# Kernel optimization log

Measured on AMD Instinct MI355X. Metric: run time of the kernel, lower is better.

Reference implementation:

```python
import jax, jax.numpy as jnp
import numpy as np

DY, DO, DI = 16, 256, 256
BS = 4096
EPS = 1e-6


def setup_inputs() -> dict:
    key = jax.random.key(0)
    k1, k2, k3, k4, k5 = jax.random.split(key, 5)
    k = 1.0 / float(np.sqrt(DY * DI))
    return {
        "x": jax.random.normal(k1, (DY * DI, BS), dtype=jnp.float32),
        "rms_params": jnp.ones((DY * DI,), dtype=jnp.float32)
        + 0.01 * jax.random.normal(k2, (DY * DI,), dtype=jnp.float32),
        "w_upper": jax.random.uniform(k3, (DY, DO, DI), minval=-k, maxval=k, dtype=jnp.float32),
        "w_lower": jax.random.uniform(k4, (DY, DO, DI), minval=-k, maxval=k, dtype=jnp.float32),
        "bias": jax.random.uniform(k5, (DY * DO,), minval=-k, maxval=k, dtype=jnp.float32),
    }


def reference(x, rms_params, w_upper, w_lower, bias):
    # x: (dy*di, bs) features-first layout, matching the torch op.
    dy, do, di = w_upper.shape
    bs = x.shape[1]
    # Per-column RMS factor (fc in the original op is shape (bs,)).
    fc = jax.lax.rsqrt(jnp.mean(x * x, axis=0) + EPS)  # (bs,)
    xn = x * rms_params[:, None] * fc[None, :]          # fused norm+scale
    xb = xn.reshape(dy, di, bs)
    # Dyadic structured matmul: upper acts on block d, lower on its paired
    # (reversed) block dy-1-d.
    up = jnp.einsum("doi,dib->dob", w_upper, xb)
    lo = jnp.einsum("doi,dib->dob", w_lower, xb[::-1])
    y = jax.nn.relu(up + lo + bias.reshape(dy, do, 1))
    return y.reshape(dy * do, bs)
```

## Files before the change

kernel.cpp:

```cpp
#include <hip/hip_runtime.h>

#define DYN 16
#define DON 256
#define DIN 256
#define BSN 4096
#define NF 4096
#define KTOT 512

typedef unsigned short u16;
typedef __attribute__((ext_vector_type(8))) short bf16x8;
typedef __attribute__((ext_vector_type(4))) float f32x4;
typedef __attribute__((ext_vector_type(4))) unsigned short u16x4;

static __device__ __forceinline__ u16 f2bf(float f) {
  unsigned u = __builtin_bit_cast(unsigned, f);
  u += 0x7fffu + ((u >> 16) & 1u);
  return (u16)(u >> 16);
}
static __device__ __forceinline__ float bf2f(u16 h) {
  unsigned u = ((unsigned)h) << 16;
  return __builtin_bit_cast(float, u);
}

__global__ __launch_bounds__(256) void k_prep_w(
    const float* __restrict__ wu, const float* __restrict__ wl,
    const float* __restrict__ rms, u16* __restrict__ aprep) {
  int e = blockIdx.x * 256 + threadIdx.x;
  int row = e >> 6;
  int k0 = (e & 63) << 3;
  int d = row >> 8;
  const float* src;
  const float* rp;
  if (k0 < 256) {
    src = wu + (size_t)row * 256 + k0;
    rp  = rms + d * 256 + k0;
  } else {
    src = wl + (size_t)row * 256 + (k0 - 256);
    rp  = rms + (DYN - 1 - d) * 256 + (k0 - 256);
  }
  float4 s0 = *reinterpret_cast<const float4*>(src);
  float4 s1 = *reinterpret_cast<const float4*>(src + 4);
  float4 r0 = *reinterpret_cast<const float4*>(rp);
  float4 r1 = *reinterpret_cast<const float4*>(rp + 4);
  bf16x8 o;
  o[0] = (short)f2bf(s0.x * r0.x); o[1] = (short)f2bf(s0.y * r0.y);
  o[2] = (short)f2bf(s0.z * r0.z); o[3] = (short)f2bf(s0.w * r0.w);
  o[4] = (short)f2bf(s1.x * r1.x); o[5] = (short)f2bf(s1.y * r1.y);
  o[6] = (short)f2bf(s1.z * r1.z); o[7] = (short)f2bf(s1.w * r1.w);
  *reinterpret_cast<bf16x8*>(aprep + (size_t)row * KTOT + k0) = o;
}

__global__ __launch_bounds__(256) void k_transpose(
    const float* __restrict__ x, u16* __restrict__ xbf,
    float* __restrict__ partial) {
  __shared__ u16 tile[128 * 132];
  const int t = threadIdx.x;
  const int bt = blockIdx.x, ft = blockIdx.y;
  const float* xb = x + (size_t)ft * 128 * BSN + bt * 128;
  const int frow = t >> 5, b4 = (t & 31) * 4;
  #pragma unroll
  for (int p = 0; p < 16; ++p) {
    int f = p * 8 + frow;
    float4 v = *reinterpret_cast<const float4*>(xb + (size_t)f * BSN + b4);
    u16x4 h;
    h[0] = f2bf(v.x); h[1] = f2bf(v.y); h[2] = f2bf(v.z); h[3] = f2bf(v.w);
    *reinterpret_cast<u16x4*>(&tile[f * 132 + b4]) = h;
  }
  __syncthreads();
  const int chunk = t & 15;
  const int bg = t >> 4;
  #pragma unroll
  for (int p = 0; p < 8; ++p) {
    int b = bg + p * 16;
    float s = 0.f;
    bf16x8 w;
    #pragma unroll
    for (int jj = 0; jj < 8; ++jj) {
      int j = (jj + chunk) & 7;
      u16 v = tile[(chunk * 8 + j) * 132 + b];
      float xv = bf2f(v);
      s += xv * xv;
      w[j] = (short)v;
    }
    *reinterpret_cast<bf16x8*>(
        xbf + (size_t)(bt * 128 + b) * NF + ft * 128 + chunk * 8) = w;
    #pragma unroll
    for (int m = 1; m < 16; m <<= 1) s += __shfl_xor(s, m, 64);
    if (chunk == 0) partial[ft * BSN + bt * 128 + b] = s;
  }
}

__global__ __launch_bounds__(256, 3) void k_gemm(
    const u16* __restrict__ aprep, const u16* __restrict__ xbf,
    const float* __restrict__ partial, const float* __restrict__ bias,
    float* __restrict__ out) {
  extern __shared__ char smem[];
  float* fcl = (float*)smem;
  u16* As = (u16*)(smem + 512);
  u16* Bs = As + 3 * 4096;
  const int bid = blockIdx.x;
  const int x8 = bid & 7, s = bid >> 3;
  const int d = (s & 1) ? (15 - x8) : x8;
  const int mt = (s >> 1) & 1;
  const int nt = s >> 2;
  const int t = threadIdx.x;
  const int wave = t >> 6, lane = t & 63;
  const int lhi = lane >> 4, llo = lane & 15;
  const int wm = wave >> 1, wn = wave & 1;
  const int arow0 = d * 256 + mt * 128;
  const int bcol0 = nt * 128;

  f32x4 acc[4][4] = {};

  auto stage = [&](int slot, int kt) {
    const int fbase = (kt < 8) ? (d * 256 + kt * 32)
                               : ((DYN - 1 - d) * 256 + (kt - 8) * 32);
    #pragma unroll
    for (int j = 0; j < 2; ++j) {
      int c = j * 256 + t;
      int cl = c ^ ((c >> 3) & 7);
      int r = cl >> 2, kc = cl & 3;
      const u16* ga = aprep + (size_t)(arow0 + r) * KTOT + kt * 32 + kc * 8;
      const u16* gb = xbf + (size_t)(bcol0 + r) * NF + fbase + kc * 8;
      unsigned lbase = (unsigned)((j * 256 + wave * 64) * 16);
      __builtin_amdgcn_global_load_lds(
          (const __attribute__((address_space(1))) unsigned int*)ga,
          (__attribute__((address_space(3))) unsigned int*)(
              (char*)&As[slot * 4096] + lbase), 16, 0, 0);
      __builtin_amdgcn_global_load_lds(
          (const __attribute__((address_space(1))) unsigned int*)gb,
          (__attribute__((address_space(3))) unsigned int*)(
              (char*)&Bs[slot * 4096] + lbase), 16, 0, 0);
    }
  };

  const int kmask = ((llo >> 1) & 7) << 4;

  stage(0, 0);
  stage(1, 1);
  if (t < 128) {
    int col = bcol0 + t;
    float fs = 0.f;
    #pragma unroll
    for (int i = 0; i < 32; ++i) fs += partial[i * BSN + col];
    fcl[t] = rsqrtf(fs * (1.0f / 4096.0f) + 1e-6f);
  }
  asm volatile("s_waitcnt vmcnt(4)\n\ts_barrier" ::: "memory");

  for (int kt = 0; kt < 16; ++kt) {
    const int slot = kt % 3;
    if (kt < 14) stage((kt + 2) % 3, kt + 2);

    bf16x8 af[4], bq[4];
    #pragma unroll
    for (int m = 0; m < 4; ++m) {
      int rowa = wm * 64 + m * 16 + llo;
      int offa = (rowa * 64 + lhi * 16) ^ kmask;
      af[m] = *reinterpret_cast<const bf16x8*>(
          (const char*)&As[slot * 4096] + offa);
    }
    #pragma unroll
    for (int n = 0; n < 4; ++n) {
      int rowb = wn * 64 + n * 16 + llo;
      int offb = (rowb * 64 + lhi * 16) ^ kmask;
      bq[n] = *reinterpret_cast<const bf16x8*>(
          (const char*)&Bs[slot * 4096] + offb);
    }
    __builtin_amdgcn_s_setprio(1);
    #pragma unroll
    for (int m = 0; m < 4; ++m)
      #pragma unroll
      for (int n = 0; n < 4; ++n)
        acc[m][n] = __builtin_amdgcn_mfma_f32_16x16x32_bf16(
            af[m], bq[n], acc[m][n], 0, 0, 0);
    __builtin_amdgcn_s_setprio(0);

    if (kt < 14) {
      asm volatile("s_waitcnt vmcnt(4)\n\ts_barrier" ::: "memory");
    } else if (kt == 14) {
      asm volatile("s_waitcnt vmcnt(0)\n\ts_barrier" ::: "memory");
    }
  }

  float fcv[4];
  #pragma unroll
  for (int n = 0; n < 4; ++n) fcv[n] = fcl[wn * 64 + n * 16 + llo];
  #pragma unroll
  for (int m = 0; m < 4; ++m) {
    int row0 = arow0 + wm * 64 + m * 16 + lhi * 4;
    float bv[4];
    #pragma unroll
    for (int r = 0; r < 4; ++r) bv[r] = bias[row0 + r];
    #pragma unroll
    for (int n = 0; n < 4; ++n) {
      int col = bcol0 + wn * 64 + n * 16 + llo;
      #pragma unroll
      for (int r = 0; r < 4; ++r) {
        float v = acc[m][n][r] * fcv[n] + bv[r];
        out[(size_t)(row0 + r) * BSN + col] = fmaxf(v, 0.f);
      }
    }
  }
}

extern "C" void kernel_launch(void* const* d_in, const int* in_sizes, int n_in,
                              void* d_out, int out_size, void* d_ws, size_t ws_size,
                              hipStream_t stream) {
  (void)in_sizes; (void)n_in; (void)out_size; (void)ws_size;
  const float* x    = (const float*)d_in[0];
  const float* rms  = (const float*)d_in[1];
  const float* wu   = (const float*)d_in[2];
  const float* wl   = (const float*)d_in[3];
  const float* bias = (const float*)d_in[4];
  float* out = (float*)d_out;

  char* ws = (char*)d_ws;
  u16* xbf      = (u16*)ws;
  u16* aprep    = (u16*)(ws + 33554432);
  float* partial = (float*)(ws + 37748736);

  k_prep_w<<<1024, 256, 0, stream>>>(wu, wl, rms, aprep);
  k_transpose<<<dim3(32, 32), 256, 0, stream>>>(x, xbf, partial);
  k_gemm<<<1024, 256, 49664, stream>>>(aprep, xbf, partial, bias, out);
}
```

Measured before the change: 57.87 us.

## Compute paired dyadic output blocks per CTA, sharing the staged x tile

Each GEMM workgroup now computes outputs for both block d and its mirror 15-d. It stages one x tile and two weight tiles per k-step, reusing the x tile across two accumulator sets. This halves x traffic per output, changes the grid from 1024 to 512 workgroups with occupancy hint 2, and enlarges LDS to triple-buffer three tiles. The epilogue is reoriented so each lane writes float4 along the batch dimension, at the cost of doubled accumulator registers.

```diff
diff --git a/kernel.cpp b/kernel.cpp
--- a/kernel.cpp
+++ b/kernel.cpp
@@ -90,115 +90,138 @@
   }
 }
 
-__global__ __launch_bounds__(256, 3) void k_gemm(
+__global__ __launch_bounds__(256, 2) void k_gemm(
     const u16* __restrict__ aprep, const u16* __restrict__ xbf,
     const float* __restrict__ partial, const float* __restrict__ bias,
     float* __restrict__ out) {
   extern __shared__ char smem[];
   float* fcl = (float*)smem;
-  u16* As = (u16*)(smem + 512);
-  u16* Bs = As + 3 * 4096;
+  u16* slots = (u16*)(smem + 512);
   const int bid = blockIdx.x;
-  const int x8 = bid & 7, s = bid >> 3;
-  const int d = (s & 1) ? (15 - x8) : x8;
-  const int mt = (s >> 1) & 1;
-  const int nt = s >> 2;
+  const int d  = bid & 7;
+  const int mt = (bid >> 3) & 1;
+  const int bt = bid >> 4;
   const int t = threadIdx.x;
   const int wave = t >> 6, lane = t & 63;
   const int lhi = lane >> 4, llo = lane & 15;
   const int wm = wave >> 1, wn = wave & 1;
-  const int arow0 = d * 256 + mt * 128;
-  const int bcol0 = nt * 128;
-
-  f32x4 acc[4][4] = {};
+  const int bb0 = bt * 128;
+  const int fr1 = d * 256 + mt * 128;
+  const int fr2 = (15 - d) * 256 + mt * 128;
+
+  f32x4 acc1[4][4] = {}, acc2[4][4] = {};
 
   auto stage = [&](int slot, int kt) {
     const int fbase = (kt < 8) ? (d * 256 + kt * 32)
-                               : ((DYN - 1 - d) * 256 + (kt - 8) * 32);
+                               : ((15 - d) * 256 + (kt - 8) * 32);
+    const int k1 = kt * 32;
+    const int k2 = (kt ^ 8) * 32;
+    char* sA  = (char*)(slots + slot * 12288);
+    char* sBd = sA + 8192;
+    char* sB2 = sA + 16384;
     #pragma unroll
     for (int j = 0; j < 2; ++j) {
       int c = j * 256 + t;
       int cl = c ^ ((c >> 3) & 7);
       int r = cl >> 2, kc = cl & 3;
-      const u16* ga = aprep + (size_t)(arow0 + r) * KTOT + kt * 32 + kc * 8;
-      const u16* gb = xbf + (size_t)(bcol0 + r) * NF + fbase + kc * 8;
       unsigned lbase = (unsigned)((j * 256 + wave * 64) * 16);
+      const u16* ga  = xbf   + (size_t)(bb0 + r) * NF   + fbase + kc * 8;
+      const u16* gbd = aprep + (size_t)(fr1 + r) * KTOT + k1 + kc * 8;
+      const u16* gb2 = aprep + (size_t)(fr2 + r) * KTOT + k2 + kc * 8;
       __builtin_amdgcn_global_load_lds(
           (const __attribute__((address_space(1))) unsigned int*)ga,
-          (__attribute__((address_space(3))) unsigned int*)(
-              (char*)&As[slot * 4096] + lbase), 16, 0, 0);
+          (__attribute__((address_space(3))) unsigned int*)(sA + lbase),
+          16, 0, 0);
       __builtin_amdgcn_global_load_lds(
-          (const __attribute__((address_space(1))) unsigned int*)gb,
-          (__attribute__((address_space(3))) unsigned int*)(
-              (char*)&Bs[slot * 4096] + lbase), 16, 0, 0);
+          (const __attribute__((address_space(1))) unsigned int*)gbd,
+          (__attribute__((address_space(3))) unsigned int*)(sBd + lbase),
+          16, 0, 0);
+      __builtin_amdgcn_global_load_lds(
+          (const __attribute__((address_space(1))) unsigned int*)gb2,
+          (__attribute__((address_space(3))) unsigned int*)(sB2 + lbase),
+          16, 0, 0);
     }
   };
 
   const int kmask = ((llo >> 1) & 7) << 4;
 
+  if (t < 128) {
+    float fs = 0.f;
+    #pragma unroll
+    for (int i = 0; i < 32; ++i) fs += partial[i * BSN + bb0 + t];
+    fcl[t] = rsqrtf(fs * (1.0f / 4096.0f) + 1e-6f);
+  }
   stage(0, 0);
   stage(1, 1);
-  if (t < 128) {
-    int col = bcol0 + t;
-    float fs = 0.f;
-    #pragma unroll
-    for (int i = 0; i < 32; ++i) fs += partial[i * BSN + col];
-    fcl[t] = rsqrtf(fs * (1.0f / 4096.0f) + 1e-6f);
-  }
-  asm volatile("s_waitcnt vmcnt(4)\n\ts_barrier" ::: "memory");
+  asm volatile("s_waitcnt vmcnt(6)\n\ts_barrier" ::: "memory");
 
   for (int kt = 0; kt < 16; ++kt) {
     const int slot = kt % 3;
     if (kt < 14) stage((kt + 2) % 3, kt + 2);
 
-    bf16x8 af[4], bq[4];
+    const char* sA  = (const char*)(slots + slot * 12288);
+    const char* sBd = sA + 8192;
+    const char* sB2 = sA + 16384;
+    bf16x8 af[4], b1[4], b2[4];
     #pragma unroll
     for (int m = 0; m < 4; ++m) {
       int rowa = wm * 64 + m * 16 + llo;
       int offa = (rowa * 64 + lhi * 16) ^ kmask;
-      af[m] = *reinterpret_cast<const bf16x8*>(
-          (const char*)&As[slot * 4096] + offa);
+      af[m] = *reinterpret_cast<const bf16x8*>(sA + offa);
     }
     #pragma unroll
     for (int n = 0; n < 4; ++n) {
       int rowb = wn * 64 + n * 16 + llo;
       int offb = (rowb * 64 + lhi * 16) ^ kmask;
-      bq[n] = *reinterpret_cast<const bf16x8*>(
-          (const char*)&Bs[slot * 4096] + offb);
+      b1[n] = *reinterpret_cast<const bf16x8*>(sBd + offb);
+      b2[n] = *reinterpret_cast<const bf16x8*>(sB2 + offb);
     }
     __builtin_amdgcn_s_setprio(1);
     #pragma unroll
     for (int m = 0; m < 4; ++m)
       #pragma unroll
       for (int n = 0; n < 4; ++n)
-        acc[m][n] = __builtin_amdgcn_mfma_f32_16x16x32_bf16(
-            af[m], bq[n], acc[m][n], 0, 0, 0);
+        acc1[m][n] = __builtin_amdgcn_mfma_f32_16x16x32_bf16(
+            af[m], b1[n], acc1[m][n], 0, 0, 0);
+    #pragma unroll
+    for (int m = 0; m < 4; ++m)
+      #pragma unroll
+      for (int n = 0; n < 4; ++n)
+        acc2[m][n] = __builtin_amdgcn_mfma_f32_16x16x32_bf16(
+            af[m], b2[n], acc2[m][n], 0, 0, 0);
     __builtin_amdgcn_s_setprio(0);
 
     if (kt < 14) {
-      asm volatile("s_waitcnt vmcnt(4)\n\ts_barrier" ::: "memory");
+      asm volatile("s_waitcnt vmcnt(6)\n\ts_barrier" ::: "memory");
     } else if (kt == 14) {
       asm volatile("s_waitcnt vmcnt(0)\n\ts_barrier" ::: "memory");
     }
   }
 
-  float fcv[4];
-  #pragma unroll
-  for (int n = 0; n < 4; ++n) fcv[n] = fcl[wn * 64 + n * 16 + llo];
-  #pragma unroll
-  for (int m = 0; m < 4; ++m) {
-    int row0 = arow0 + wm * 64 + m * 16 + lhi * 4;
-    float bv[4];
-    #pragma unroll
-    for (int r = 0; r < 4; ++r) bv[r] = bias[row0 + r];
-    #pragma unroll
-    for (int n = 0; n < 4; ++n) {
-      int col = bcol0 + wn * 64 + n * 16 + llo;
+  float4 fcq[4];
+  #pragma unroll
+  for (int m = 0; m < 4; ++m)
+    fcq[m] = *reinterpret_cast<const float4*>(&fcl[wm * 64 + m * 16 + lhi * 4]);
+  const int bbase = bb0 + wm * 64 + lhi * 4;
+  #pragma unroll
+  for (int n = 0; n < 4; ++n) {
+    int f1 = fr1 + wn * 64 + n * 16 + llo;
+    int f2 = fr2 + wn * 64 + n * 16 + llo;
+    float bv1 = bias[f1], bv2 = bias[f2];
+    #pragma unroll
+    for (int m = 0; m < 4; ++m) {
+      float4 v1, v2;
       #pragma unroll
       for (int r = 0; r < 4; ++r) {
-        float v = acc[m][n][r] * fcv[n] + bv[r];
-        out[(size_t)(row0 + r) * BSN + col] = fmaxf(v, 0.f);
+        float fcr = (r == 0) ? fcq[m].x : (r == 1) ? fcq[m].y
+                    : (r == 2) ? fcq[m].z : fcq[m].w;
+        float a1 = acc1[m][n][r] * fcr + bv1;
+        float a2 = acc2[m][n][r] * fcr + bv2;
+        ((float*)&v1)[r] = fmaxf(a1, 0.f);
+        ((float*)&v2)[r] = fmaxf(a2, 0.f);
       }
+      *reinterpret_cast<float4*>(out + (size_t)f1 * BSN + bbase + m * 16) = v1;
+      *reinterpret_cast<float4*>(out + (size_t)f2 * BSN + bbase + m * 16) = v2;
     }
   }
 }
@@ -221,5 +244,5 @@
 
   k_prep_w<<<1024, 256, 0, stream>>>(wu, wl, rms, aprep);
   k_transpose<<<dim3(32, 32), 256, 0, stream>>>(x, xbf, partial);
-  k_gemm<<<1024, 256, 49664, stream>>>(aprep, xbf, partial, bias, out);
-}
+  k_gemm<<<512, 256, 74240, stream>>>(aprep, xbf, partial, bias, out);
+}
```

After: 59.64 us. 3.1% more time.

## Keep full weight tile resident in LDS and stream activations from global

Applied to the files above, without the earlier changes.

Merges the weight-prep and transpose kernels into one launch. Restructures the GEMM so each block loads its whole 64x512 weight slab into LDS once and streams bf16 activation fragments straight from global memory into registers, covering 512 batch columns per block with a transposed output tile that allows float4 stores. This removes the per-k-step staging of both operands and the barriers around it, but activation loads are no longer pipelined through LDS. It also lowers occupancy to two blocks per CU with a larger LDS footprint.

```diff
diff --git a/kernel.cpp b/kernel.cpp
--- a/kernel.cpp
+++ b/kernel.cpp
@@ -22,40 +22,41 @@
   return __builtin_bit_cast(float, u);
 }
 
-__global__ __launch_bounds__(256) void k_prep_w(
-    const float* __restrict__ wu, const float* __restrict__ wl,
-    const float* __restrict__ rms, u16* __restrict__ aprep) {
-  int e = blockIdx.x * 256 + threadIdx.x;
-  int row = e >> 6;
-  int k0 = (e & 63) << 3;
-  int d = row >> 8;
-  const float* src;
-  const float* rp;
-  if (k0 < 256) {
-    src = wu + (size_t)row * 256 + k0;
-    rp  = rms + d * 256 + k0;
-  } else {
-    src = wl + (size_t)row * 256 + (k0 - 256);
-    rp  = rms + (DYN - 1 - d) * 256 + (k0 - 256);
-  }
-  float4 s0 = *reinterpret_cast<const float4*>(src);
-  float4 s1 = *reinterpret_cast<const float4*>(src + 4);
-  float4 r0 = *reinterpret_cast<const float4*>(rp);
-  float4 r1 = *reinterpret_cast<const float4*>(rp + 4);
-  bf16x8 o;
-  o[0] = (short)f2bf(s0.x * r0.x); o[1] = (short)f2bf(s0.y * r0.y);
-  o[2] = (short)f2bf(s0.z * r0.z); o[3] = (short)f2bf(s0.w * r0.w);
-  o[4] = (short)f2bf(s1.x * r1.x); o[5] = (short)f2bf(s1.y * r1.y);
-  o[6] = (short)f2bf(s1.z * r1.z); o[7] = (short)f2bf(s1.w * r1.w);
-  *reinterpret_cast<bf16x8*>(aprep + (size_t)row * KTOT + k0) = o;
-}
-
-__global__ __launch_bounds__(256) void k_transpose(
-    const float* __restrict__ x, u16* __restrict__ xbf,
+__global__ __launch_bounds__(256) void k_pre(
+    const float* __restrict__ x, const float* __restrict__ wu,
+    const float* __restrict__ wl, const float* __restrict__ rms,
+    u16* __restrict__ aprep, u16* __restrict__ xbf,
     float* __restrict__ partial) {
   __shared__ u16 tile[128 * 132];
   const int t = threadIdx.x;
-  const int bt = blockIdx.x, ft = blockIdx.y;
+  if (blockIdx.x < 1024) {
+    int e = blockIdx.x * 256 + t;
+    int row = e >> 6;
+    int k0 = (e & 63) << 3;
+    int d = row >> 8;
+    const float* src;
+    const float* rp;
+    if (k0 < 256) {
+      src = wu + (size_t)row * 256 + k0;
+      rp  = rms + d * 256 + k0;
+    } else {
+      src = wl + (size_t)row * 256 + (k0 - 256);
+      rp  = rms + (DYN - 1 - d) * 256 + (k0 - 256);
+    }
+    float4 s0 = *reinterpret_cast<const float4*>(src);
+    float4 s1 = *reinterpret_cast<const float4*>(src + 4);
+    float4 r0 = *reinterpret_cast<const float4*>(rp);
+    float4 r1 = *reinterpret_cast<const float4*>(rp + 4);
+    bf16x8 o;
+    o[0] = (short)f2bf(s0.x * r0.x); o[1] = (short)f2bf(s0.y * r0.y);
+    o[2] = (short)f2bf(s0.z * r0.z); o[3] = (short)f2bf(s0.w * r0.w);
+    o[4] = (short)f2bf(s1.x * r1.x); o[5] = (short)f2bf(s1.y * r1.y);
+    o[6] = (short)f2bf(s1.z * r1.z); o[7] = (short)f2bf(s1.w * r1.w);
+    *reinterpret_cast<bf16x8*>(aprep + (size_t)row * KTOT + k0) = o;
+    return;
+  }
+  const int bid = blockIdx.x - 1024;
+  const int bt = bid & 31, ft = bid >> 5;
   const float* xb = x + (size_t)ft * 128 * BSN + bt * 128;
   const int frow = t >> 5, b4 = (t & 31) * 4;
   #pragma unroll
@@ -90,114 +91,112 @@
   }
 }
 
-__global__ __launch_bounds__(256, 3) void k_gemm(
+__global__ __launch_bounds__(256, 2) void k_gemm(
     const u16* __restrict__ aprep, const u16* __restrict__ xbf,
     const float* __restrict__ partial, const float* __restrict__ bias,
     float* __restrict__ out) {
   extern __shared__ char smem[];
-  float* fcl = (float*)smem;
-  u16* As = (u16*)(smem + 512);
-  u16* Bs = As + 3 * 4096;
+  u16* Wlds = (u16*)smem;
+  float* fcl = (float*)(smem + 65536);
   const int bid = blockIdx.x;
-  const int x8 = bid & 7, s = bid >> 3;
-  const int d = (s & 1) ? (15 - x8) : x8;
-  const int mt = (s >> 1) & 1;
-  const int nt = s >> 2;
+  const int dp = bid & 7;
+  const int r6 = bid >> 3;
+  const int bt = r6 & 7;
+  const int sub = r6 >> 3;
+  const int wrow0 = (sub < 4) ? dp * 256 + sub * 64
+                              : (15 - dp) * 256 + (sub - 4) * 64;
+  const int dblk = wrow0 >> 8;
+  const int oblk = 15 - dblk;
+  const int b0 = bt * 512;
   const int t = threadIdx.x;
   const int wave = t >> 6, lane = t & 63;
   const int lhi = lane >> 4, llo = lane & 15;
-  const int wm = wave >> 1, wn = wave & 1;
-  const int arow0 = d * 256 + mt * 128;
-  const int bcol0 = nt * 128;
-
-  f32x4 acc[4][4] = {};
-
-  auto stage = [&](int slot, int kt) {
-    const int fbase = (kt < 8) ? (d * 256 + kt * 32)
-                               : ((DYN - 1 - d) * 256 + (kt - 8) * 32);
-    #pragma unroll
-    for (int j = 0; j < 2; ++j) {
-      int c = j * 256 + t;
+  const int wb0 = wave * 128;
+
+  #pragma unroll
+  for (int s = 0; s < 4; ++s) {
+    int kt = wave * 4 + s;
+    #pragma unroll
+    for (int j = 0; j < 4; ++j) {
+      int c = j * 64 + lane;
       int cl = c ^ ((c >> 3) & 7);
-      int r = cl >> 2, kc = cl & 3;
-      const u16* ga = aprep + (size_t)(arow0 + r) * KTOT + kt * 32 + kc * 8;
-      const u16* gb = xbf + (size_t)(bcol0 + r) * NF + fbase + kc * 8;
-      unsigned lbase = (unsigned)((j * 256 + wave * 64) * 16);
+      int r = cl >> 2, ko = cl & 3;
+      const u16* g = aprep + (size_t)(wrow0 + r) * KTOT + kt * 32 + ko * 8;
       __builtin_amdgcn_global_load_lds(
-          (const __attribute__((address_space(1))) unsigned int*)ga,
+          (const __attribute__((address_space(1))) unsigned int*)g,
           (__attribute__((address_space(3))) unsigned int*)(
-              (char*)&As[slot * 4096] + lbase), 16, 0, 0);
-      __builtin_amdgcn_global_load_lds(
-          (const __attribute__((address_space(1))) unsigned int*)gb,
-          (__attribute__((address_space(3))) unsigned int*)(
-              (char*)&Bs[slot * 4096] + lbase), 16, 0, 0);
-    }
-  };
+              smem + kt * 4096 + j * 1024), 16, 0, 0);
+    }
+  }
+  #pragma unroll
+  for (int h = 0; h < 2; ++h) {
+    int lb = h * 256 + t;
+    float fs = 0.f;
+    #pragma unroll
+    for (int i = 0; i < 32; ++i) fs += partial[i * BSN + b0 + lb];
+    fcl[lb] = rsqrtf(fs * (1.0f / 4096.0f) + 1e-6f);
+  }
+  asm volatile("s_waitcnt vmcnt(0) lgkmcnt(0)\n\ts_barrier" ::: "memory");
 
   const int kmask = ((llo >> 1) & 7) << 4;
-
-  stage(0, 0);
-  stage(1, 1);
-  if (t < 128) {
-    int col = bcol0 + t;
-    float fs = 0.f;
-    #pragma unroll
-    for (int i = 0; i < 32; ++i) fs += partial[i * BSN + col];
-    fcl[t] = rsqrtf(fs * (1.0f / 4096.0f) + 1e-6f);
-  }
-  asm volatile("s_waitcnt vmcnt(4)\n\ts_barrier" ::: "memory");
-
-  for (int kt = 0; kt < 16; ++kt) {
-    const int slot = kt % 3;
-    if (kt < 14) stage((kt + 2) % 3, kt + 2);
-
-    bf16x8 af[4], bq[4];
-    #pragma unroll
-    for (int m = 0; m < 4; ++m) {
-      int rowa = wm * 64 + m * 16 + llo;
-      int offa = (rowa * 64 + lhi * 16) ^ kmask;
-      af[m] = *reinterpret_cast<const bf16x8*>(
-          (const char*)&As[slot * 4096] + offa);
-    }
-    #pragma unroll
-    for (int n = 0; n < 4; ++n) {
-      int rowb = wn * 64 + n * 16 + llo;
-      int offb = (rowb * 64 + lhi * 16) ^ kmask;
-      bq[n] = *reinterpret_cast<const bf16x8*>(
-          (const char*)&Bs[slot * 4096] + offb);
-    }
-    __builtin_amdgcn_s_setprio(1);
-    #pragma unroll
-    for (int m = 0; m < 4; ++m)
-      #pragma unroll
-      for (int n = 0; n < 4; ++n)
-        acc[m][n] = __builtin_amdgcn_mfma_f32_16x16x32_bf16(
-            af[m], bq[n], acc[m][n], 0, 0, 0);
-    __builtin_amdgcn_s_setprio(0);
-
-    if (kt < 14) {
-      asm volatile("s_waitcnt vmcnt(4)\n\ts_barrier" ::: "memory");
-    } else if (kt == 14) {
-      asm volatile("s_waitcnt vmcnt(0)\n\ts_barrier" ::: "memory");
-    }
-  }
-
-  float fcv[4];
-  #pragma unroll
-  for (int n = 0; n < 4; ++n) fcv[n] = fcl[wn * 64 + n * 16 + llo];
-  #pragma unroll
-  for (int m = 0; m < 4; ++m) {
-    int row0 = arow0 + wm * 64 + m * 16 + lhi * 4;
-    float bv[4];
-    #pragma unroll
-    for (int r = 0; r < 4; ++r) bv[r] = bias[row0 + r];
-    #pragma unroll
-    for (int n = 0; n < 4; ++n) {
-      int col = bcol0 + wn * 64 + n * 16 + llo;
-      #pragma unroll
-      for (int r = 0; r < 4; ++r) {
-        float v = acc[m][n][r] * fcv[n] + bv[r];
-        out[(size_t)(row0 + r) * BSN + col] = fmaxf(v, 0.f);
+  f32x4 acc[4][2][4] = {};
+
+  #pragma unroll
+  for (int p = 0; p < 8; ++p) {
+    bf16x8 wf[2][4];
+    #pragma unroll
+    for (int q = 0; q < 2; ++q) {
+      int kt = p * 2 + q;
+      #pragma unroll
+      for (int n = 0; n < 4; ++n) {
+        int off = kt * 4096 + ((((n * 16 + llo) * 64) + lhi * 16) ^ kmask);
+        wf[q][n] = *reinterpret_cast<const bf16x8*>((const char*)Wlds + off);
+      }
+    }
+    #pragma unroll
+    for (int bs = 0; bs < 4; ++bs) {
+      bf16x8 af[2][2];
+      #pragma unroll
+      for (int q = 0; q < 2; ++q) {
+        int kt = p * 2 + q;
+        int f = (kt < 8) ? (dblk * 256 + kt * 32 + lhi * 8)
+                         : (oblk * 256 + (kt - 8) * 32 + lhi * 8);
+        #pragma unroll
+        for (int bm = 0; bm < 2; ++bm) {
+          int b = b0 + wb0 + bs * 32 + bm * 16 + llo;
+          af[q][bm] = *reinterpret_cast<const bf16x8*>(
+              xbf + (size_t)b * NF + f);
+        }
+      }
+      __builtin_amdgcn_s_setprio(1);
+      #pragma unroll
+      for (int q = 0; q < 2; ++q)
+        #pragma unroll
+        for (int bm = 0; bm < 2; ++bm)
+          #pragma unroll
+          for (int n = 0; n < 4; ++n)
+            acc[bs][bm][n] = __builtin_amdgcn_mfma_f32_16x16x32_bf16(
+                af[q][bm], wf[q][n], acc[bs][bm][n], 0, 0, 0);
+      __builtin_amdgcn_s_setprio(0);
+    }
+  }
+
+  #pragma unroll
+  for (int bs = 0; bs < 4; ++bs) {
+    #pragma unroll
+    for (int bm = 0; bm < 2; ++bm) {
+      int lb = wb0 + bs * 32 + bm * 16 + lhi * 4;
+      float4 fq = *reinterpret_cast<const float4*>(&fcl[lb]);
+      #pragma unroll
+      for (int n = 0; n < 4; ++n) {
+        int fo = wrow0 + n * 16 + llo;
+        float bv = bias[fo];
+        float4 v;
+        v.x = fmaxf(acc[bs][bm][n][0] * fq.x + bv, 0.f);
+        v.y = fmaxf(acc[bs][bm][n][1] * fq.y + bv, 0.f);
+        v.z = fmaxf(acc[bs][bm][n][2] * fq.z + bv, 0.f);
+        v.w = fmaxf(acc[bs][bm][n][3] * fq.w + bv, 0.f);
+        *reinterpret_cast<float4*>(out + (size_t)fo * BSN + b0 + lb) = v;
       }
     }
   }
@@ -219,7 +218,6 @@
   u16* aprep    = (u16*)(ws + 33554432);
   float* partial = (float*)(ws + 37748736);
 
-  k_prep_w<<<1024, 256, 0, stream>>>(wu, wl, rms, aprep);
-  k_transpose<<<dim3(32, 32), 256, 0, stream>>>(x, xbf, partial);
-  k_gemm<<<1024, 256, 49664, stream>>>(aprep, xbf, partial, bias, out);
-}
+  k_pre<<<2048, 256, 0, stream>>>(x, wu, wl, rms, aprep, xbf, partial);
+  k_gemm<<<512, 256, 67584, stream>>>(aprep, xbf, partial, bias, out);
+}
```

Measured after the change: 70.30 us. 21.5% more time.
